# Optimization experiments

Measured on AMD Instinct MI355X. Metric: run time of the kernel, lower is better.

The kernel has to match this reference:

```python
import jax, jax.numpy as jnp
import numpy as np

NUM_JOINT = 31
BATCH = 131072
# parent index per joint (-1 = root); parents always precede children (topological order)
PARENTS = (-1, 0, 1, 2, 3, 4,
           0, 6, 7, 8, 9,
           0, 11, 12, 13, 14,
           13, 16, 17, 18, 19,
           13, 21, 22, 23, 24,
           13, 26, 27, 28, 29)


def setup_inputs() -> dict:
    key = jax.random.key(0)
    k1, k2, k3, k4 = jax.random.split(key, 4)
    root_position = jax.random.normal(k1, (BATCH, 3), dtype=jnp.float32)
    joint = jax.random.normal(k2, (BATCH, NUM_JOINT * 4), dtype=jnp.float32)
    fake_bone_length = jax.random.uniform(k3, (BATCH, NUM_JOINT), dtype=jnp.float32)
    # skeleton offsets: identity 4x4 with a random bone-offset translation in [:3,3]
    offs = jnp.broadcast_to(jnp.eye(4, dtype=jnp.float32), (NUM_JOINT, 4, 4))
    offs = offs.at[:, :3, 3].set(jax.random.normal(k4, (NUM_JOINT, 3), dtype=jnp.float32))
    return {"root_position": root_position, "joint": joint,
            "fake_bone_length": fake_bone_length, "offsets": offs}


def quaternion_to_matrix(q):
    # q: [..., 4] with (w, x, y, z); pytorch3d-style (normalizes via 2/|q|^2)
    w, x, y, z = q[..., 0], q[..., 1], q[..., 2], q[..., 3]
    two_s = 2.0 / jnp.sum(q * q, axis=-1)
    r00 = 1.0 - two_s * (y * y + z * z)
    r01 = two_s * (x * y - z * w)
    r02 = two_s * (x * z + y * w)
    r10 = two_s * (x * y + z * w)
    r11 = 1.0 - two_s * (x * x + z * z)
    r12 = two_s * (y * z - x * w)
    r20 = two_s * (x * z - y * w)
    r21 = two_s * (y * z + x * w)
    r22 = 1.0 - two_s * (x * x + y * y)
    R = jnp.stack([r00, r01, r02, r10, r11, r12, r20, r21, r22], axis=-1)
    return R.reshape(q.shape[:-1] + (3, 3))


def reference(root_position, joint, fake_bone_length, offsets):
    B = joint.shape[0]
    J = NUM_JOINT
    quats = joint.reshape(B, J, 4)
    R3 = quaternion_to_matrix(quats)                              # [B,J,3,3]
    # embed rotation into homogeneous 4x4
    R4 = jnp.zeros((B, J, 4, 4), dtype=joint.dtype)
    R4 = R4.at[..., :3, :3].set(R3).at[..., 3, 3].set(1.0)
    # offset translation matrices, translation scaled by fake bone length
    trans = offsets[None, :, :3, 3] * fake_bone_length[:, :, None]  # [B,J,3]
    T = jnp.broadcast_to(offsets[None], (B, J, 4, 4)).at[:, :, :3, 3].set(trans)
    RT = jnp.matmul(R4, T)                                        # [B,J,4,4]
    # root translation matrix from root_position * 100
    root_T = jnp.broadcast_to(jnp.eye(4, dtype=joint.dtype), (B, 4, 4))
    root_T = root_T.at[:, :3, 3].set(root_position * 100.0)
    # walk the tree in topological order (fixed small structural loop)
    mats = [None] * J
    mats[0] = jnp.matmul(root_T, RT[:, 0])
    for j in range(1, J):
        mats[j] = jnp.matmul(mats[PARENTS[j]], RT[:, j])
    joint_coordinates = jnp.stack(mats, axis=1)                   # [B,J,4,4]
    # transpose(jc,2,3)[:, j, 3, :] == jc[:, j, :, 3] (homogeneous position column)
    fake_positions = joint_coordinates[:, :, :, 3]                # [B,J,4]
    return fake_positions
```

## Files before the change

### kernel.cpp

```cpp
#include <hip/hip_runtime.h>

constexpr int NJ = 31;
constexpr int ROWS = 64;
constexpr int JF = NJ * 4;

struct M34 {
    float r[9];
    float t[3];
};

__device__ __forceinline__ void make_RT(int j, float4 q, float len,
                                        const float* __restrict__ offs,
                                        float Rr[9], float Rt[3]) {
    const float w = q.x, x = q.y, y = q.z, z = q.w;
    const float two_s = 2.0f / (w * w + x * x + y * y + z * z);
    float R[9];
    R[0] = 1.0f - two_s * (y * y + z * z);
    R[1] = two_s * (x * y - z * w);
    R[2] = two_s * (x * z + y * w);
    R[3] = two_s * (x * y + z * w);
    R[4] = 1.0f - two_s * (x * x + z * z);
    R[5] = two_s * (y * z - x * w);
    R[6] = two_s * (x * z - y * w);
    R[7] = two_s * (y * z + x * w);
    R[8] = 1.0f - two_s * (x * x + y * y);

    const float4* O4 = reinterpret_cast<const float4*>(offs) + (size_t)j * 4;
    const float4 o0 = O4[0], o1 = O4[1], o2 = O4[2];
    const float O[12] = {o0.x, o0.y, o0.z, o1.x, o1.y, o1.z, o2.x, o2.y, o2.z,
                         o0.w * len, o1.w * len, o2.w * len};
#pragma unroll
    for (int r = 0; r < 3; ++r) {
#pragma unroll
        for (int c = 0; c < 3; ++c) {
            Rr[r * 3 + c] = R[r * 3 + 0] * O[0 + c] +
                            R[r * 3 + 1] * O[3 + c] +
                            R[r * 3 + 2] * O[6 + c];
        }
        Rt[r] = R[r * 3 + 0] * O[9] + R[r * 3 + 1] * O[10] + R[r * 3 + 2] * O[11];
    }
}

__device__ __forceinline__ M34 compose(const M34& P, const float Rr[9],
                                       const float Rt[3]) {
    M34 C;
#pragma unroll
    for (int r = 0; r < 3; ++r) {
#pragma unroll
        for (int c = 0; c < 3; ++c) {
            C.r[r * 3 + c] = P.r[r * 3 + 0] * Rr[0 * 3 + c] +
                             P.r[r * 3 + 1] * Rr[1 * 3 + c] +
                             P.r[r * 3 + 2] * Rr[2 * 3 + c];
        }
        C.t[r] = P.r[r * 3 + 0] * Rt[0] + P.r[r * 3 + 1] * Rt[1] +
                 P.r[r * 3 + 2] * Rt[2] + P.t[r];
    }
    return C;
}

__global__ __launch_bounds__(256) void fk_layer_kernel(
    const float* __restrict__ root_position,
    const float* __restrict__ joint,
    const float* __restrict__ fbl,
    const float* __restrict__ offsets,
    float* __restrict__ out) {
    __shared__ float so[ROWS * JF];

    const int tid = threadIdx.x;
    const int r = tid >> 2;
    const int c = tid & 3;
    const int cc = c < 2 ? c : 2;
    const int rowBase = blockIdx.x * ROWS;
    const size_t b = (size_t)(rowBase + r);

    const float4* jq = reinterpret_cast<const float4*>(joint + b * JF);
    float4 q0 = jq[0];
    float4 qa[5], qb[5];
#pragma unroll
    for (int s = 0; s < 5; ++s) qa[s] = jq[1 + 5 * cc + s];
#pragma unroll
    for (int s = 0; s < 5; ++s) qb[s] = jq[16 + 5 * cc + s];

    const float* fr = fbl + b * NJ;
    const float f0 = fr[0];
    float fa[5], fb_[5];
#pragma unroll
    for (int s = 0; s < 5; ++s) fa[s] = fr[1 + 5 * cc + s];
#pragma unroll
    for (int s = 0; s < 5; ++s) fb_[s] = fr[16 + 5 * cc + s];

    const float rx = root_position[b * 3 + 0] * 100.0f;
    const float ry = root_position[b * 3 + 1] * 100.0f;
    const float rz = root_position[b * 3 + 2] * 100.0f;

    float* srow = so + r * JF;

    M34 M0;
    {
        float Rr[9], Rt[3];
        make_RT(0, q0, f0, offsets, Rr, Rt);
#pragma unroll
        for (int i = 0; i < 9; ++i) M0.r[i] = Rr[i];
        M0.t[0] = Rt[0] + rx;
        M0.t[1] = Rt[1] + ry;
        M0.t[2] = Rt[2] + rz;
        if (c == 0)
            *reinterpret_cast<float4*>(&srow[0]) =
                make_float4(M0.t[0], M0.t[1], M0.t[2], 1.0f);
    }

    M34 cur = M0, M13 = M0;
    {
        const int jb = 1 + 5 * cc;
#pragma unroll
        for (int s = 0; s < 5; ++s) {
            const int j = jb + s;
            float Rr[9], Rt[3];
            make_RT(j, qa[s], fa[s], offsets, Rr, Rt);
            cur = compose(cur, Rr, Rt);
            if (c < 3)
                *reinterpret_cast<float4*>(&srow[j * 4]) =
                    make_float4(cur.t[0], cur.t[1], cur.t[2], 1.0f);
            if (s == 2) M13 = cur;
        }
    }

    const int wlane = tid & 63;
    const int src = (wlane & ~3) | 2;
#pragma unroll
    for (int i = 0; i < 9; ++i) M13.r[i] = __shfl(M13.r[i], src, 64);
#pragma unroll
    for (int i = 0; i < 3; ++i) M13.t[i] = __shfl(M13.t[i], src, 64);

    cur = M13;
    {
        const int jb = 16 + 5 * cc;
#pragma unroll
        for (int s = 0; s < 5; ++s) {
            const int j = jb + s;
            float Rr[9], Rt[3];
            make_RT(j, qb[s], fb_[s], offsets, Rr, Rt);
            cur = compose(cur, Rr, Rt);
            if (c < 3)
                *reinterpret_cast<float4*>(&srow[j * 4]) =
                    make_float4(cur.t[0], cur.t[1], cur.t[2], 1.0f);
        }
    }

    __syncthreads();

    const float4* s4 = reinterpret_cast<const float4*>(so);
    float4* gout = reinterpret_cast<float4*>(out + (size_t)rowBase * JF);
#pragma unroll
    for (int ch = 0; ch < 8; ++ch) {
        const int idx = ch * 256 + tid;
        if (idx < ROWS * NJ) gout[idx] = s4[idx];
    }
}

extern "C" void kernel_launch(void* const* d_in, const int* in_sizes, int n_in,
                              void* d_out, int out_size, void* d_ws, size_t ws_size,
                              hipStream_t stream) {
    const float* root = (const float*)d_in[0];
    const float* joint = (const float*)d_in[1];
    const float* fblp = (const float*)d_in[2];
    const float* offs = (const float*)d_in[3];
    float* out = (float*)d_out;

    const int B = in_sizes[0] / 3;
    fk_layer_kernel<<<B / ROWS, 256, 0, stream>>>(root, joint, fblp, offs, out);
}
```

Before: 33.93 us.

## Double-buffer input tiles into LDS with async global_load_lds across multiple tiles per block

Each block now handles four 32-row tiles in sequence with 128 threads. Quaternion and bone-length tiles are staged straight into shared memory with global_load_lds, and the next tile is prefetched into a second buffer while the current one is computed. The quaternion buffer is reused in place to hold output positions before they are copied out. The aim is to overlap global loads with compute and get coalesced input reads. In exchange the grid is smaller with fewer threads per block, there are extra barriers per tile, and correctness depends on implicit waits for the async loads at the barriers.

```diff
diff --git a/kernel.cpp b/kernel.cpp
--- a/kernel.cpp
+++ b/kernel.cpp
@@ -1,8 +1,14 @@
 #include <hip/hip_runtime.h>
 
 constexpr int NJ = 31;
-constexpr int ROWS = 64;
+constexpr int ROWS = 32;
+constexpr int TPB = 128;
+constexpr int TILES_PER_BLK = 4;
 constexpr int JF = NJ * 4;
+constexpr int QREAL = ROWS * JF * 4;
+constexpr int QPAD = 16384;
+constexpr int FREAL = ROWS * NJ * 4;
+constexpr int FPAD = 4096;
 
 struct M34 {
     float r[9];
@@ -58,103 +64,133 @@
     return C;
 }
 
-__global__ __launch_bounds__(256) void fk_layer_kernel(
+__global__ __launch_bounds__(TPB) void fk_layer_kernel(
     const float* __restrict__ root_position,
     const float* __restrict__ joint,
     const float* __restrict__ fbl,
     const float* __restrict__ offsets,
     float* __restrict__ out) {
-    __shared__ float so[ROWS * JF];
+    __shared__ float qbuf[2][QPAD / 4];
+    __shared__ float fbuf[2][FPAD / 4];
 
     const int tid = threadIdx.x;
+    const int wave = tid >> 6;
+    const int lane = tid & 63;
     const int r = tid >> 2;
     const int c = tid & 3;
     const int cc = c < 2 ? c : 2;
-    const int rowBase = blockIdx.x * ROWS;
-    const size_t b = (size_t)(rowBase + r);
-
-    const float4* jq = reinterpret_cast<const float4*>(joint + b * JF);
-    float4 q0 = jq[0];
-    float4 qa[5], qb[5];
-#pragma unroll
-    for (int s = 0; s < 5; ++s) qa[s] = jq[1 + 5 * cc + s];
-#pragma unroll
-    for (int s = 0; s < 5; ++s) qb[s] = jq[16 + 5 * cc + s];
-
-    const float* fr = fbl + b * NJ;
-    const float f0 = fr[0];
-    float fa[5], fb_[5];
-#pragma unroll
-    for (int s = 0; s < 5; ++s) fa[s] = fr[1 + 5 * cc + s];
-#pragma unroll
-    for (int s = 0; s < 5; ++s) fb_[s] = fr[16 + 5 * cc + s];
-
-    const float rx = root_position[b * 3 + 0] * 100.0f;
-    const float ry = root_position[b * 3 + 1] * 100.0f;
-    const float rz = root_position[b * 3 + 2] * 100.0f;
-
-    float* srow = so + r * JF;
-
-    M34 M0;
-    {
-        float Rr[9], Rt[3];
-        make_RT(0, q0, f0, offsets, Rr, Rt);
-#pragma unroll
-        for (int i = 0; i < 9; ++i) M0.r[i] = Rr[i];
-        M0.t[0] = Rt[0] + rx;
-        M0.t[1] = Rt[1] + ry;
-        M0.t[2] = Rt[2] + rz;
-        if (c == 0)
-            *reinterpret_cast<float4*>(&srow[0]) =
-                make_float4(M0.t[0], M0.t[1], M0.t[2], 1.0f);
-    }
-
-    M34 cur = M0, M13 = M0;
-    {
-        const int jb = 1 + 5 * cc;
-#pragma unroll
-        for (int s = 0; s < 5; ++s) {
-            const int j = jb + s;
+
+    const int tile0 = blockIdx.x * TILES_PER_BLK;
+
+    auto stage = [&](int bi, int tile) {
+        const char* qsrc = (const char*)(joint + (size_t)tile * ROWS * JF);
+        char* qdst = (char*)&qbuf[bi][0];
+#pragma unroll
+        for (int i = 0; i < 8; ++i) {
+            const int chunk = i * 2 + wave;
+            int off = chunk * 1024 + lane * 16;
+            if (off > QREAL - 16) off = QREAL - 16;
+            __builtin_amdgcn_global_load_lds(
+                (const __attribute__((address_space(1))) unsigned int*)(qsrc + off),
+                (__attribute__((address_space(3))) unsigned int*)(qdst + chunk * 1024),
+                16, 0, 0);
+        }
+        const char* fsrc = (const char*)(fbl + (size_t)tile * ROWS * NJ);
+        char* fdst = (char*)&fbuf[bi][0];
+#pragma unroll
+        for (int i = 0; i < 2; ++i) {
+            const int chunk = i * 2 + wave;
+            int off = chunk * 1024 + lane * 16;
+            if (off > FREAL - 16) off = FREAL - 16;
+            __builtin_amdgcn_global_load_lds(
+                (const __attribute__((address_space(1))) unsigned int*)(fsrc + off),
+                (__attribute__((address_space(3))) unsigned int*)(fdst + chunk * 1024),
+                16, 0, 0);
+        }
+    };
+
+    stage(0, tile0);
+    __syncthreads();
+
+    for (int it = 0; it < TILES_PER_BLK; ++it) {
+        const int cur = it & 1;
+        const int tile = tile0 + it;
+
+        if (it + 1 < TILES_PER_BLK) stage(cur ^ 1, tile + 1);
+
+        const size_t b = (size_t)tile * ROWS + r;
+        const float rx = root_position[b * 3 + 0] * 100.0f;
+        const float ry = root_position[b * 3 + 1] * 100.0f;
+        const float rz = root_position[b * 3 + 2] * 100.0f;
+
+        float* srow = &qbuf[cur][r * JF];
+        const float* frow = &fbuf[cur][r * NJ];
+
+        M34 M0;
+        {
+            float4 q = *reinterpret_cast<const float4*>(&srow[0]);
             float Rr[9], Rt[3];
-            make_RT(j, qa[s], fa[s], offsets, Rr, Rt);
-            cur = compose(cur, Rr, Rt);
-            if (c < 3)
-                *reinterpret_cast<float4*>(&srow[j * 4]) =
-                    make_float4(cur.t[0], cur.t[1], cur.t[2], 1.0f);
-            if (s == 2) M13 = cur;
-        }
-    }
-
-    const int wlane = tid & 63;
-    const int src = (wlane & ~3) | 2;
-#pragma unroll
-    for (int i = 0; i < 9; ++i) M13.r[i] = __shfl(M13.r[i], src, 64);
-#pragma unroll
-    for (int i = 0; i < 3; ++i) M13.t[i] = __shfl(M13.t[i], src, 64);
-
-    cur = M13;
-    {
-        const int jb = 16 + 5 * cc;
-#pragma unroll
-        for (int s = 0; s < 5; ++s) {
-            const int j = jb + s;
-            float Rr[9], Rt[3];
-            make_RT(j, qb[s], fb_[s], offsets, Rr, Rt);
-            cur = compose(cur, Rr, Rt);
-            if (c < 3)
-                *reinterpret_cast<float4*>(&srow[j * 4]) =
-                    make_float4(cur.t[0], cur.t[1], cur.t[2], 1.0f);
-        }
-    }
-
-    __syncthreads();
-
-    const float4* s4 = reinterpret_cast<const float4*>(so);
-    float4* gout = reinterpret_cast<float4*>(out + (size_t)rowBase * JF);
-#pragma unroll
-    for (int ch = 0; ch < 8; ++ch) {
-        const int idx = ch * 256 + tid;
-        if (idx < ROWS * NJ) gout[idx] = s4[idx];
+            make_RT(0, q, frow[0], offsets, Rr, Rt);
+#pragma unroll
+            for (int i = 0; i < 9; ++i) M0.r[i] = Rr[i];
+            M0.t[0] = Rt[0] + rx;
+            M0.t[1] = Rt[1] + ry;
+            M0.t[2] = Rt[2] + rz;
+            if (c == 0)
+                *reinterpret_cast<float4*>(&srow[0]) =
+                    make_float4(M0.t[0], M0.t[1], M0.t[2], 1.0f);
+        }
+
+        M34 cur_m = M0, M13 = M0;
+        {
+            const int jb = 1 + 5 * cc;
+#pragma unroll
+            for (int s = 0; s < 5; ++s) {
+                const int j = jb + s;
+                float4 q = *reinterpret_cast<const float4*>(&srow[j * 4]);
+                float Rr[9], Rt[3];
+                make_RT(j, q, frow[j], offsets, Rr, Rt);
+                cur_m = compose(cur_m, Rr, Rt);
+                if (c < 3)
+                    *reinterpret_cast<float4*>(&srow[j * 4]) =
+                        make_float4(cur_m.t[0], cur_m.t[1], cur_m.t[2], 1.0f);
+                if (s == 2) M13 = cur_m;
+            }
+        }
+
+        const int src = (lane & ~3) | 2;
+#pragma unroll
+        for (int i = 0; i < 9; ++i) M13.r[i] = __shfl(M13.r[i], src, 64);
+#pragma unroll
+        for (int i = 0; i < 3; ++i) M13.t[i] = __shfl(M13.t[i], src, 64);
+
+        cur_m = M13;
+        {
+            const int jb = 16 + 5 * cc;
+#pragma unroll
+            for (int s = 0; s < 5; ++s) {
+                const int j = jb + s;
+                float4 q = *reinterpret_cast<const float4*>(&srow[j * 4]);
+                float Rr[9], Rt[3];
+                make_RT(j, q, frow[j], offsets, Rr, Rt);
+                cur_m = compose(cur_m, Rr, Rt);
+                if (c < 3)
+                    *reinterpret_cast<float4*>(&srow[j * 4]) =
+                        make_float4(cur_m.t[0], cur_m.t[1], cur_m.t[2], 1.0f);
+            }
+        }
+
+        __syncthreads();
+
+        const float4* s4 = reinterpret_cast<const float4*>(&qbuf[cur][0]);
+        float4* gout = reinterpret_cast<float4*>(out + (size_t)tile * ROWS * JF);
+#pragma unroll
+        for (int ch = 0; ch < 8; ++ch) {
+            const int idx = ch * TPB + tid;
+            if (idx < QREAL / 16) gout[idx] = s4[idx];
+        }
+
+        __syncthreads();
     }
 }
 
@@ -168,5 +204,7 @@
     float* out = (float*)d_out;
 
     const int B = in_sizes[0] / 3;
-    fk_layer_kernel<<<B / ROWS, 256, 0, stream>>>(root, joint, fblp, offs, out);
-}
+    const int tiles = B / ROWS;
+    fk_layer_kernel<<<tiles / TILES_PER_BLK, TPB, 0, stream>>>(root, joint, fblp,
+                                                              offs, out);
+}
```

New measurement: 37.25 us. +9.8%, slower.
